# Kernel optimization log

Measured on AMD Instinct MI355X. Metric: run time of the kernel, lower is better.

Reference implementation:

```python
import jax, jax.numpy as jnp
import numpy as np

H = 2048
E = 64
TOP_K = 4
EPS = 1e-6


def _rms_norm(x, eps):
    # Gemma RMSNorm without scale: compute in fp32, cast back.
    x32 = x.astype(jnp.float32)
    var = jnp.mean(x32 * x32, axis=-1, keepdims=True)
    return (x32 * jax.lax.rsqrt(var + eps)).astype(x.dtype)


def setup_inputs() -> dict:
    key = jax.random.key(0)
    k1, k2 = jax.random.split(key)
    hidden_states = jax.random.normal(k1, (4, 4096, H), dtype=jnp.float32)
    proj_w = jax.random.normal(k2, (E, H), dtype=jnp.float32) * (H ** -0.5)
    scale = jnp.ones((H,), dtype=jnp.float32)
    per_expert_scale = jnp.ones((E,), dtype=jnp.float32)
    return {"hidden_states": hidden_states, "proj_w": proj_w,
            "scale": scale, "per_expert_scale": per_expert_scale}


def reference(hidden_states, proj_w, scale, per_expert_scale):
    scalar_root_size = H ** (-0.5)
    h = _rms_norm(hidden_states, EPS) * scale * scalar_root_size  # [B,S,H]
    expert_scores = jnp.einsum('bsh,eh->bse', h, proj_w)          # [B,S,E]
    router_probabilities = jax.nn.softmax(expert_scores, axis=-1)
    top_k_weights, top_k_index = jax.lax.top_k(router_probabilities, TOP_K)
    top_k_weights = top_k_weights / jnp.sum(top_k_weights, axis=-1, keepdims=True)
    top_k_weights = top_k_weights * per_expert_scale[top_k_index]
    return router_probabilities, top_k_weights, top_k_index
```

## Files before the change

### kernel.cpp

```cpp
#include <hip/hip_runtime.h>
#include <cstddef>

#define HDIM 2048
#define NE 64
#define TOPK 4

typedef short bf16x8 __attribute__((ext_vector_type(8)));
typedef float f32x4 __attribute__((ext_vector_type(4)));

__device__ __forceinline__ void split3(float a, unsigned short& h0,
                                       unsigned short& h1, unsigned short& h2) {
    unsigned int u = __float_as_uint(a);
    h0 = (unsigned short)(u >> 16);
    float f0 = __uint_as_float(u & 0xffff0000u);
    float r1 = a - f0;
    unsigned int v = __float_as_uint(r1);
    h1 = (unsigned short)(v >> 16);
    float f1 = __uint_as_float(v & 0xffff0000u);
    float r2 = r1 - f1;
    h2 = (unsigned short)(__float_as_uint(r2) >> 16);
}

__global__ __launch_bounds__(256) void prep_b_kernel(
    const float* __restrict__ w, const float* __restrict__ scale,
    unsigned short* __restrict__ wtb)
{
    const int s = blockIdx.x;
    const int n = threadIdx.x >> 6;
    const int l = threadIdx.x & 63;
    const int e = 16 * n + (l & 15);
    const int k = 32 * s + 8 * (l >> 4);
    unsigned short h0[8], h1[8], h2[8];
    #pragma unroll
    for (int j = 0; j < 8; ++j) {
        float v = w[(size_t)e * HDIM + k + j] * scale[k + j];
        split3(v, h0[j], h1[j], h2[j]);
    }
    size_t off = ((size_t)s * 4 + n) * 512 + (size_t)l * 8;
    #pragma unroll
    for (int j = 0; j < 8; ++j) {
        wtb[off + j]          = h0[j];
        wtb[131072 + off + j] = h1[j];
        wtb[262144 + off + j] = h2[j];
    }
}

__global__ __launch_bounds__(256, 2) void fused_router_kernel(
    const float* __restrict__ x, const unsigned short* __restrict__ wtb,
    const float* __restrict__ pes,
    float* __restrict__ probs, float* __restrict__ tkw, float* __restrict__ tki)
{
    __shared__ float Sp[4][32 * 65];
    __shared__ float SQp[4][32];
    __shared__ float Sl[32 * 65];
    __shared__ float Pl[32 * 65];
    __shared__ float FN[32];
    __shared__ float RS[32];

    const int tid = threadIdx.x;
    const int kh = tid >> 6;
    const int l = tid & 63;
    const int tok0 = blockIdx.x * 32;
    const int m = l & 15;
    const int g = l >> 4;

    const float* xr0 = x + (size_t)(tok0 + m) * HDIM + 512 * kh + 8 * g;
    const float* xr1 = xr0 + (size_t)16 * HDIM;
    const unsigned short* wb = wtb + (size_t)(16 * kh) * 2048 + (size_t)l * 8;

    f32x4 acc0[4], acc1[4];
    #pragma unroll
    for (int n = 0; n < 4; ++n) {
        acc0[n] = (f32x4){0.f, 0.f, 0.f, 0.f};
        acc1[n] = (f32x4){0.f, 0.f, 0.f, 0.f};
    }
    float ssq0 = 0.f, ssq1 = 0.f;

    float4 Aq[2][4];
    bf16x8 Bb[2][12];

#define LOADA(buf, s) { \
        Aq[buf][0] = *(const float4*)(xr0 + 32 * (s)); \
        Aq[buf][1] = *(const float4*)(xr0 + 32 * (s) + 4); \
        Aq[buf][2] = *(const float4*)(xr1 + 32 * (s)); \
        Aq[buf][3] = *(const float4*)(xr1 + 32 * (s) + 4); }
#define LOADB(buf, s) { \
        const unsigned short* bs_ = wb + (size_t)(s) * 2048; \
        _Pragma("unroll") \
        for (int n = 0; n < 4; ++n) { \
            Bb[buf][3*n + 0] = *(const bf16x8*)(bs_ + n * 512); \
            Bb[buf][3*n + 1] = *(const bf16x8*)(bs_ + n * 512 + 131072); \
            Bb[buf][3*n + 2] = *(const bf16x8*)(bs_ + n * 512 + 262144); } }

    LOADA(0, 0);
    LOADB(0, 0);

    #pragma unroll
    for (int s = 0; s < 16; ++s) {
        const int cur = s & 1, nxt = cur ^ 1;
        if (s + 1 < 16) { LOADA(nxt, s + 1); LOADB(nxt, s + 1); }

        float af0[8], af1[8];
        *(float4*)af0 = Aq[cur][0]; *(float4*)(af0 + 4) = Aq[cur][1];
        *(float4*)af1 = Aq[cur][2]; *(float4*)(af1 + 4) = Aq[cur][3];
        unsigned short p0[8], p1[8], p2[8], q0[8], q1[8], q2[8];
        #pragma unroll
        for (int j = 0; j < 8; ++j) {
            split3(af0[j], p0[j], p1[j], p2[j]);
            split3(af1[j], q0[j], q1[j], q2[j]);
            ssq0 = fmaf(af0[j], af0[j], ssq0);
            ssq1 = fmaf(af1[j], af1[j], ssq1);
        }
        bf16x8 a0, a1, a2, c0, c1, c2;
        #pragma unroll
        for (int j = 0; j < 8; ++j) {
            a0[j] = (short)p0[j]; a1[j] = (short)p1[j]; a2[j] = (short)p2[j];
            c0[j] = (short)q0[j]; c1[j] = (short)q1[j]; c2[j] = (short)q2[j];
        }
        #pragma unroll
        for (int n = 0; n < 4; ++n) {
            bf16x8 b0 = Bb[cur][3*n + 0];
            bf16x8 b1 = Bb[cur][3*n + 1];
            bf16x8 b2 = Bb[cur][3*n + 2];
            acc0[n] = __builtin_amdgcn_mfma_f32_16x16x32_bf16(a0, b0, acc0[n], 0, 0, 0);
            acc0[n] = __builtin_amdgcn_mfma_f32_16x16x32_bf16(a0, b1, acc0[n], 0, 0, 0);
            acc0[n] = __builtin_amdgcn_mfma_f32_16x16x32_bf16(a1, b0, acc0[n], 0, 0, 0);
            acc0[n] = __builtin_amdgcn_mfma_f32_16x16x32_bf16(a1, b1, acc0[n], 0, 0, 0);
            acc0[n] = __builtin_amdgcn_mfma_f32_16x16x32_bf16(a0, b2, acc0[n], 0, 0, 0);
            acc0[n] = __builtin_amdgcn_mfma_f32_16x16x32_bf16(a2, b0, acc0[n], 0, 0, 0);
            acc1[n] = __builtin_amdgcn_mfma_f32_16x16x32_bf16(c0, b0, acc1[n], 0, 0, 0);
            acc1[n] = __builtin_amdgcn_mfma_f32_16x16x32_bf16(c0, b1, acc1[n], 0, 0, 0);
            acc1[n] = __builtin_amdgcn_mfma_f32_16x16x32_bf16(c1, b0, acc1[n], 0, 0, 0);
            acc1[n] = __builtin_amdgcn_mfma_f32_16x16x32_bf16(c1, b1, acc1[n], 0, 0, 0);
            acc1[n] = __builtin_amdgcn_mfma_f32_16x16x32_bf16(c0, b2, acc1[n], 0, 0, 0);
            acc1[n] = __builtin_amdgcn_mfma_f32_16x16x32_bf16(c2, b0, acc1[n], 0, 0, 0);
        }
    }
#undef LOADA
#undef LOADB

    ssq0 += __shfl_xor(ssq0, 16, 64);
    ssq0 += __shfl_xor(ssq0, 32, 64);
    ssq1 += __shfl_xor(ssq1, 16, 64);
    ssq1 += __shfl_xor(ssq1, 32, 64);

    #pragma unroll
    for (int n = 0; n < 4; ++n)
        #pragma unroll
        for (int r = 0; r < 4; ++r) {
            Sp[kh][(4 * g + r) * 65 + 16 * n + m]      = acc0[n][r];
            Sp[kh][(16 + 4 * g + r) * 65 + 16 * n + m] = acc1[n][r];
        }
    if (l < 16) {
        SQp[kh][m]      = ssq0;
        SQp[kh][16 + m] = ssq1;
    }
    __syncthreads();

    if (tid < 32) {
        float st = (SQp[0][tid] + SQp[1][tid]) + (SQp[2][tid] + SQp[3][tid]);
        FN[tid] = rsqrtf(st * (1.0f / HDIM) + 1e-6f) * 0.022097086912079612f;
    }
    __syncthreads();

    #pragma unroll
    for (int qq = 0; qq < 2; qq++) {
        int f = tid + 256 * qq;
        int mr = f >> 4;
        int e4 = (f & 15) * 4;
        float4 t0 = *(const float4*)&Sp[0][mr * 65 + e4];
        float4 t1 = *(const float4*)&Sp[1][mr * 65 + e4];
        float4 t2 = *(const float4*)&Sp[2][mr * 65 + e4];
        float4 t3 = *(const float4*)&Sp[3][mr * 65 + e4];
        float fn = FN[mr];
        Sl[mr * 65 + e4 + 0] = ((t0.x + t1.x) + (t2.x + t3.x)) * fn;
        Sl[mr * 65 + e4 + 1] = ((t0.y + t1.y) + (t2.y + t3.y)) * fn;
        Sl[mr * 65 + e4 + 2] = ((t0.z + t1.z) + (t2.z + t3.z)) * fn;
        Sl[mr * 65 + e4 + 3] = ((t0.w + t1.w) + (t2.w + t3.w)) * fn;
    }
    __syncthreads();

    if (tid < 32) {
        const int mm = tid;
        float mx = -3.0e38f;
        for (int e = 0; e < NE; e++) mx = fmaxf(mx, Sl[mm * 65 + e]);
        float sum = 0.f;
        for (int e = 0; e < NE; e++) {
            float p = __expf(Sl[mm * 65 + e] - mx);
            Pl[mm * 65 + e] = p;
            sum += p;
        }
        RS[mm] = 1.0f / sum;
    }
    __syncthreads();

    #pragma unroll
    for (int qq = 0; qq < 2; qq++) {
        int f = tid + 256 * qq;
        int mr = f >> 4;
        int e0 = (f & 15) * 4;
        float rs = RS[mr];
        float4 pv;
        pv.x = Pl[mr * 65 + e0 + 0] * rs;
        pv.y = Pl[mr * 65 + e0 + 1] * rs;
        pv.z = Pl[mr * 65 + e0 + 2] * rs;
        pv.w = Pl[mr * 65 + e0 + 3] * rs;
        *(float4*)&probs[(size_t)(tok0 + mr) * NE + e0] = pv;
    }

    if (tid < 32) {
        const int mm = tid;
        float wvv[TOPK]; int idx[TOPK];
        float wsum = 0.f;
        #pragma unroll
        for (int kk = 0; kk < TOPK; ++kk) {
            float best = -3.0e38f; int bi = 0;
            for (int e = 0; e < NE; e++) {
                float v = Sl[mm * 65 + e];
                if (v > best) { best = v; bi = e; }
            }
            Sl[mm * 65 + bi] = -3.4e38f;
            float p = Pl[mm * 65 + bi];
            wvv[kk] = p; idx[kk] = bi; wsum += p;
        }
        float inv = 1.0f / wsum;
        size_t ob = (size_t)(tok0 + mm) * TOPK;
        #pragma unroll
        for (int kk = 0; kk < TOPK; kk++) {
            tkw[ob + kk] = wvv[kk] * inv * pes[idx[kk]];
            tki[ob + kk] = (float)idx[kk];
        }
    }
}

extern "C" void kernel_launch(void* const* d_in, const int* in_sizes, int n_in,
                              void* d_out, int out_size, void* d_ws, size_t ws_size,
                              hipStream_t stream) {
    const float* x     = (const float*)d_in[0];
    const float* w     = (const float*)d_in[1];
    const float* scale = (const float*)d_in[2];
    const float* pes   = (const float*)d_in[3];
    const int tokens = in_sizes[0] / HDIM;

    float* probs = (float*)d_out;
    float* tkw   = probs + (size_t)tokens * NE;
    float* tki   = tkw + (size_t)tokens * TOPK;

    unsigned short* wtb = (unsigned short*)d_ws;

    prep_b_kernel<<<HDIM / 32, 256, 0, stream>>>(w, scale, wtb);

    const int grid = tokens / 32;
    fused_router_kernel<<<grid, 256, 0, stream>>>(x, wtb, pes, probs, tkw, tki);
}
```

Baseline: 47.53 us.

## Replace three-way bf16 split GEMM with two-way fp16 hi/lo split

```diff
diff --git a/kernel.cpp b/kernel.cpp
--- a/kernel.cpp
+++ b/kernel.cpp
@@ -5,20 +5,21 @@
 #define NE 64
 #define TOPK 4
 
-typedef short bf16x8 __attribute__((ext_vector_type(8)));
+typedef short short8 __attribute__((ext_vector_type(8)));
 typedef float f32x4 __attribute__((ext_vector_type(4)));
 
-__device__ __forceinline__ void split3(float a, unsigned short& h0,
-                                       unsigned short& h1, unsigned short& h2) {
-    unsigned int u = __float_as_uint(a);
-    h0 = (unsigned short)(u >> 16);
-    float f0 = __uint_as_float(u & 0xffff0000u);
-    float r1 = a - f0;
-    unsigned int v = __float_as_uint(r1);
-    h1 = (unsigned short)(v >> 16);
-    float f1 = __uint_as_float(v & 0xffff0000u);
-    float r2 = r1 - f1;
-    h2 = (unsigned short)(__float_as_uint(r2) >> 16);
+__device__ __forceinline__ void split2u(float a, unsigned short& h0, unsigned short& h1) {
+    _Float16 x0 = (_Float16)a;
+    float r = a - (float)x0;
+    _Float16 x1 = (_Float16)(r * 4096.0f);
+    h0 = __builtin_bit_cast(unsigned short, x0);
+    h1 = __builtin_bit_cast(unsigned short, x1);
+}
+
+__device__ __forceinline__ f32x4 mfma_f16(short8 a, short8 b, f32x4 c) {
+    typedef _Float16 f16x8_t __attribute__((ext_vector_type(8)));
+    return __builtin_amdgcn_mfma_f32_16x16x32_f16(
+        __builtin_bit_cast(f16x8_t, a), __builtin_bit_cast(f16x8_t, b), c, 0, 0, 0);
 }
 
 __global__ __launch_bounds__(256) void prep_b_kernel(
@@ -30,30 +31,28 @@
     const int l = threadIdx.x & 63;
     const int e = 16 * n + (l & 15);
     const int k = 32 * s + 8 * (l >> 4);
-    unsigned short h0[8], h1[8], h2[8];
+    unsigned short h0[8], h1[8];
     #pragma unroll
     for (int j = 0; j < 8; ++j) {
         float v = w[(size_t)e * HDIM + k + j] * scale[k + j];
-        split3(v, h0[j], h1[j], h2[j]);
+        split2u(v, h0[j], h1[j]);
     }
     size_t off = ((size_t)s * 4 + n) * 512 + (size_t)l * 8;
     #pragma unroll
     for (int j = 0; j < 8; ++j) {
         wtb[off + j]          = h0[j];
         wtb[131072 + off + j] = h1[j];
-        wtb[262144 + off + j] = h2[j];
-    }
-}
-
-__global__ __launch_bounds__(256, 2) void fused_router_kernel(
+    }
+}
+
+__global__ __launch_bounds__(256) void fused_router_kernel(
     const float* __restrict__ x, const unsigned short* __restrict__ wtb,
     const float* __restrict__ pes,
     float* __restrict__ probs, float* __restrict__ tkw, float* __restrict__ tki)
 {
     __shared__ float Sp[4][32 * 65];
+    __shared__ float Pl[32 * 65];
     __shared__ float SQp[4][32];
-    __shared__ float Sl[32 * 65];
-    __shared__ float Pl[32 * 65];
     __shared__ float FN[32];
     __shared__ float RS[32];
 
@@ -68,16 +67,18 @@
     const float* xr1 = xr0 + (size_t)16 * HDIM;
     const unsigned short* wb = wtb + (size_t)(16 * kh) * 2048 + (size_t)l * 8;
 
-    f32x4 acc0[4], acc1[4];
+    f32x4 accH0[4], accL0[4], accH1[4], accL1[4];
     #pragma unroll
     for (int n = 0; n < 4; ++n) {
-        acc0[n] = (f32x4){0.f, 0.f, 0.f, 0.f};
-        acc1[n] = (f32x4){0.f, 0.f, 0.f, 0.f};
+        accH0[n] = (f32x4){0.f, 0.f, 0.f, 0.f};
+        accL0[n] = (f32x4){0.f, 0.f, 0.f, 0.f};
+        accH1[n] = (f32x4){0.f, 0.f, 0.f, 0.f};
+        accL1[n] = (f32x4){0.f, 0.f, 0.f, 0.f};
     }
     float ssq0 = 0.f, ssq1 = 0.f;
 
     float4 Aq[2][4];
-    bf16x8 Bb[2][12];
+    short8 Bb[2][8];
 
 #define LOADA(buf, s) { \
         Aq[buf][0] = *(const float4*)(xr0 + 32 * (s)); \
@@ -88,9 +89,8 @@
         const unsigned short* bs_ = wb + (size_t)(s) * 2048; \
         _Pragma("unroll") \
         for (int n = 0; n < 4; ++n) { \
-            Bb[buf][3*n + 0] = *(const bf16x8*)(bs_ + n * 512); \
-            Bb[buf][3*n + 1] = *(const bf16x8*)(bs_ + n * 512 + 131072); \
-            Bb[buf][3*n + 2] = *(const bf16x8*)(bs_ + n * 512 + 262144); } }
+            Bb[buf][2*n + 0] = *(const short8*)(bs_ + n * 512); \
+            Bb[buf][2*n + 1] = *(const short8*)(bs_ + n * 512 + 131072); } }
 
     LOADA(0, 0);
     LOADB(0, 0);
@@ -103,38 +103,33 @@
         float af0[8], af1[8];
         *(float4*)af0 = Aq[cur][0]; *(float4*)(af0 + 4) = Aq[cur][1];
         *(float4*)af1 = Aq[cur][2]; *(float4*)(af1 + 4) = Aq[cur][3];
-        unsigned short p0[8], p1[8], p2[8], q0[8], q1[8], q2[8];
+        unsigned short p0[8], p1[8], q0[8], q1[8];
         #pragma unroll
         for (int j = 0; j < 8; ++j) {
-            split3(af0[j], p0[j], p1[j], p2[j]);
-            split3(af1[j], q0[j], q1[j], q2[j]);
+            split2u(af0[j], p0[j], p1[j]);
+            split2u(af1[j], q0[j], q1[j]);
             ssq0 = fmaf(af0[j], af0[j], ssq0);
             ssq1 = fmaf(af1[j], af1[j], ssq1);
         }
-        bf16x8 a0, a1, a2, c0, c1, c2;
+        short8 a0, a1, c0, c1;
         #pragma unroll
         for (int j = 0; j < 8; ++j) {
-            a0[j] = (short)p0[j]; a1[j] = (short)p1[j]; a2[j] = (short)p2[j];
-            c0[j] = (short)q0[j]; c1[j] = (short)q1[j]; c2[j] = (short)q2[j];
-        }
+            a0[j] = (short)p0[j]; a1[j] = (short)p1[j];
+            c0[j] = (short)q0[j]; c1[j] = (short)q1[j];
+        }
+        __builtin_amdgcn_s_setprio(1);
         #pragma unroll
         for (int n = 0; n < 4; ++n) {
-            bf16x8 b0 = Bb[cur][3*n + 0];
-            bf16x8 b1 = Bb[cur][3*n + 1];
-            bf16x8 b2 = Bb[cur][3*n + 2];
-            acc0[n] = __builtin_amdgcn_mfma_f32_16x16x32_bf16(a0, b0, acc0[n], 0, 0, 0);
-            acc0[n] = __builtin_amdgcn_mfma_f32_16x16x32_bf16(a0, b1, acc0[n], 0, 0, 0);
-            acc0[n] = __builtin_amdgcn_mfma_f32_16x16x32_bf16(a1, b0, acc0[n], 0, 0, 0);
-            acc0[n] = __builtin_amdgcn_mfma_f32_16x16x32_bf16(a1, b1, acc0[n], 0, 0, 0);
-            acc0[n] = __builtin_amdgcn_mfma_f32_16x16x32_bf16(a0, b2, acc0[n], 0, 0, 0);
-            acc0[n] = __builtin_amdgcn_mfma_f32_16x16x32_bf16(a2, b0, acc0[n], 0, 0, 0);
-            acc1[n] = __builtin_amdgcn_mfma_f32_16x16x32_bf16(c0, b0, acc1[n], 0, 0, 0);
-            acc1[n] = __builtin_amdgcn_mfma_f32_16x16x32_bf16(c0, b1, acc1[n], 0, 0, 0);
-            acc1[n] = __builtin_amdgcn_mfma_f32_16x16x32_bf16(c1, b0, acc1[n], 0, 0, 0);
-            acc1[n] = __builtin_amdgcn_mfma_f32_16x16x32_bf16(c1, b1, acc1[n], 0, 0, 0);
-            acc1[n] = __builtin_amdgcn_mfma_f32_16x16x32_bf16(c0, b2, acc1[n], 0, 0, 0);
-            acc1[n] = __builtin_amdgcn_mfma_f32_16x16x32_bf16(c2, b0, acc1[n], 0, 0, 0);
-        }
+            short8 b0 = Bb[cur][2*n + 0];
+            short8 b1 = Bb[cur][2*n + 1];
+            accH0[n] = mfma_f16(a0, b0, accH0[n]);
+            accL0[n] = mfma_f16(a0, b1, accL0[n]);
+            accL0[n] = mfma_f16(a1, b0, accL0[n]);
+            accH1[n] = mfma_f16(c0, b0, accH1[n]);
+            accL1[n] = mfma_f16(c0, b1, accL1[n]);
+            accL1[n] = mfma_f16(c1, b0, accL1[n]);
+        }
+        __builtin_amdgcn_s_setprio(0);
     }
 #undef LOADA
 #undef LOADB
@@ -144,12 +139,13 @@
     ssq1 += __shfl_xor(ssq1, 16, 64);
     ssq1 += __shfl_xor(ssq1, 32, 64);
 
+    const float LSC = 1.0f / 4096.0f;
     #pragma unroll
     for (int n = 0; n < 4; ++n)
         #pragma unroll
         for (int r = 0; r < 4; ++r) {
-            Sp[kh][(4 * g + r) * 65 + 16 * n + m]      = acc0[n][r];
-            Sp[kh][(16 + 4 * g + r) * 65 + 16 * n + m] = acc1[n][r];
+            Sp[kh][(4 * g + r) * 65 + 16 * n + m]      = fmaf(accL0[n][r], LSC, accH0[n][r]);
+            Sp[kh][(16 + 4 * g + r) * 65 + 16 * n + m] = fmaf(accL1[n][r], LSC, accH1[n][r]);
         }
     if (l < 16) {
         SQp[kh][m]      = ssq0;
@@ -158,8 +154,8 @@
     __syncthreads();
 
     if (tid < 32) {
-        float st = (SQp[0][tid] + SQp[1][tid]) + (SQp[2][tid] + SQp[3][tid]);
-        FN[tid] = rsqrtf(st * (1.0f / HDIM) + 1e-6f) * 0.022097086912079612f;
+        float q0 = (SQp[0][tid] + SQp[1][tid]) + (SQp[2][tid] + SQp[3][tid]);
+        FN[tid] = rsqrtf(q0 * (1.0f / HDIM) + 1e-6f) * 0.022097086912079612f;
     }
     __syncthreads();
 
@@ -168,17 +164,22 @@
         int f = tid + 256 * qq;
         int mr = f >> 4;
         int e4 = (f & 15) * 4;
-        float4 t0 = *(const float4*)&Sp[0][mr * 65 + e4];
-        float4 t1 = *(const float4*)&Sp[1][mr * 65 + e4];
-        float4 t2 = *(const float4*)&Sp[2][mr * 65 + e4];
-        float4 t3 = *(const float4*)&Sp[3][mr * 65 + e4];
+        int base = mr * 65 + e4;
+        float4 t0 = *(const float4*)&Sp[0][base];
+        float4 t1 = *(const float4*)&Sp[1][base];
+        float4 t2 = *(const float4*)&Sp[2][base];
+        float4 t3 = *(const float4*)&Sp[3][base];
         float fn = FN[mr];
-        Sl[mr * 65 + e4 + 0] = ((t0.x + t1.x) + (t2.x + t3.x)) * fn;
-        Sl[mr * 65 + e4 + 1] = ((t0.y + t1.y) + (t2.y + t3.y)) * fn;
-        Sl[mr * 65 + e4 + 2] = ((t0.z + t1.z) + (t2.z + t3.z)) * fn;
-        Sl[mr * 65 + e4 + 3] = ((t0.w + t1.w) + (t2.w + t3.w)) * fn;
-    }
-    __syncthreads();
+        float4 sv;
+        sv.x = ((t0.x + t1.x) + (t2.x + t3.x)) * fn;
+        sv.y = ((t0.y + t1.y) + (t2.y + t3.y)) * fn;
+        sv.z = ((t0.z + t1.z) + (t2.z + t3.z)) * fn;
+        sv.w = ((t0.w + t1.w) + (t2.w + t3.w)) * fn;
+        *(float4*)&Sp[0][base] = sv;
+    }
+    __syncthreads();
+
+    float* Sl = &Sp[0][0];
 
     if (tid < 32) {
         const int mm = tid;
```

Measured after the change: 41.35 us (median of 2 runs). -13.0%, faster.
